# Optimization experiments

Measured on AMD Instinct MI355X. Metric: run time of the kernel, lower is better.

Reference implementation:

```python
import jax, jax.numpy as jnp
from jax import lax
import numpy as np

P = 4        # pool_size
NH = 8       # nhead
EPS = 1e-5


def _maxpool(x):
    return lax.reduce_window(x, -jnp.inf, lax.max, (1, 1, P, P), (1, 1, P, P), 'VALID')


def _ln_c(x, g, b):
    # LayerNorm over channel dim of NCHW (torch applies it on NHWC last dim)
    m = x.mean(1, keepdims=True)
    v = x.var(1, keepdims=True)
    return g[None, :, None, None] * (x - m) / jnp.sqrt(v + EPS) + b[None, :, None, None]


def _dwbn(x, w, g, b, rm, rv):
    # depthwise 3x3 conv (groups=C, no bias) + BatchNorm2d (inference, running stats)
    C = x.shape[1]
    y = lax.conv_general_dilated(x, w, (1, 1), ((1, 1), (1, 1)),
                                 dimension_numbers=('NCHW', 'OIHW', 'NCHW'),
                                 feature_group_count=C)
    sc = g / jnp.sqrt(rv + EPS)
    return sc[None, :, None, None] * (y - rm[None, :, None, None]) + b[None, :, None, None]


def _heads(x):
    # n (nhead d) h w -> n (h w) nhead d
    B, C, H, W = x.shape
    return x.reshape(B, NH, C // NH, H * W).transpose(0, 3, 1, 2)


def _fuse(x, m, merge_w, mlp_w1, mlp_w2, ln2_g, ln2_b):
    # merge linear -> reshape to pooled map -> bilinear upsample x4 -> concat -> MLP -> LN -> residual
    B, C, H, W = x.shape
    m = jnp.einsum('nlh d -> nlhd', m) if False else m  # no-op, keep m as [B,L,NH,dim]
    m = m.reshape(B, -1, C) @ merge_w.T                  # [B, L, C]
    m = m.reshape(B, H // P, W // P, C).transpose(0, 3, 1, 2)
    m = jax.image.resize(m, (B, C, H, W), method='bilinear')  # align_corners=False convention
    z = jnp.concatenate([x, m], axis=1).transpose(0, 2, 3, 1)  # NHWC, 2C
    z = jax.nn.relu(z @ mlp_w1.T) @ mlp_w2.T                   # [B,H,W,C]
    mu = z.mean(-1, keepdims=True)
    var = z.var(-1, keepdims=True)
    z = ln2_g * (z - mu) / jnp.sqrt(var + EPS) + ln2_b
    return x + z.transpose(0, 3, 1, 2)


def setup_inputs() -> dict:
    key = jax.random.key(0)
    ks = jax.random.split(key, 20)
    B, C, H, W = 4, 256, 128, 128
    s = 0.05
    return {
        'x1': jax.random.normal(ks[0], (B, C, H, W), jnp.float32),
        'x2': jax.random.normal(ks[1], (B, C, H, W), jnp.float32),
        'qk_w': jax.random.normal(ks[2], (C, 1, 3, 3), jnp.float32) * s,
        'qk_g': 1.0 + 0.1 * jax.random.normal(ks[3], (C,), jnp.float32),
        'qk_b': 0.1 * jax.random.normal(ks[4], (C,), jnp.float32),
        'qk_m': 0.1 * jax.random.normal(ks[5], (C,), jnp.float32),
        'qk_v': jax.random.uniform(ks[6], (C,), jnp.float32, 0.5, 1.5),
        'v_w': jax.random.normal(ks[7], (C, 1, 3, 3), jnp.float32) * s,
        'v_g': 1.0 + 0.1 * jax.random.normal(ks[8], (C,), jnp.float32),
        'v_b': 0.1 * jax.random.normal(ks[9], (C,), jnp.float32),
        'v_m': 0.1 * jax.random.normal(ks[10], (C,), jnp.float32),
        'v_v': jax.random.uniform(ks[11], (C,), jnp.float32, 0.5, 1.5),
        'ln1_g': 1.0 + 0.1 * jax.random.normal(ks[12], (C,), jnp.float32),
        'ln1_b': 0.1 * jax.random.normal(ks[13], (C,), jnp.float32),
        'ln2_g': 1.0 + 0.1 * jax.random.normal(ks[14], (C,), jnp.float32),
        'ln2_b': 0.1 * jax.random.normal(ks[15], (C,), jnp.float32),
        'merge_w': jax.random.normal(ks[16], (C, C), jnp.float32) * s,
        'mlp_w1': jax.random.normal(ks[17], (2 * C, 2 * C), jnp.float32) * s,
        'mlp_w2': jax.random.normal(ks[18], (C, 2 * C), jnp.float32) * s,
    }


def reference(x1, x2, qk_w, qk_g, qk_b, qk_m, qk_v, v_w, v_g, v_b, v_m, v_v,
              ln1_g, ln1_b, ln2_g, ln2_b, merge_w, mlp_w1, mlp_w2):
    # pooled + normalized features (norm1 shared across q/k/v branches)
    p1 = _ln_c(_maxpool(x1), ln1_g, ln1_b)
    p2 = _ln_c(_maxpool(x2), ln1_g, ln1_b)
    query = _heads(_dwbn(p1, qk_w, qk_g, qk_b, qk_m, qk_v))  # [B,L,NH,d]
    key = _heads(_dwbn(p2, qk_w, qk_g, qk_b, qk_m, qk_v))    # [B,S,NH,d]
    v1h = _heads(_dwbn(p1, v_w, v_g, v_b, v_m, v_v))
    v2h = _heads(_dwbn(p2, v_w, v_g, v_b, v_m, v_v))
    QK = jnp.einsum('nlhd,nshd->nlsh', query, key).astype(jnp.float32)
    t = 1.0 / np.sqrt(query.shape[-1]).astype(np.float32)
    S1 = jax.nn.softmax(t * QK, axis=2)   # softmax over s (keys)
    S2 = jax.nn.softmax(t * QK, axis=3)   # softmax over head dim (as in source)
    m1 = jnp.einsum('nlsh,nshd->nlhd', S1, v2h)
    m2 = jnp.einsum('nlsh,nlhd->nshd', S2, v1h)
    out1 = _fuse(x1, m1, merge_w, mlp_w1, mlp_w2, ln2_g, ln2_b)
    out2 = _fuse(x2, m2, merge_w, mlp_w1, mlp_w2, ln2_g, ln2_b)
    return (out1, out2)
```

## Files before the change

### kernel.cpp

```cpp
#include <hip/hip_runtime.h>
#include <hip/hip_bf16.h>

#define NB 4
#define NC 256
#define NH_ 8
#define LPOOL 1024
constexpr float EPSV = 1e-5f;

typedef unsigned short ushort_t;
typedef __attribute__((ext_vector_type(8))) short bf16x8;
typedef __attribute__((ext_vector_type(4))) float f32x4;

#define OFF_P   0u
#define OFF_V2T 1048576u
#define OFF_Q   2097152u
#define OFF_K   3145728u
#define OFF_V1  4194304u
#define OFF_V2  5242880u
#define OFF_M1  6291456u
#define OFF_M2  7340032u
#define OFF_MG  8388608u
#define OFF_A   9437184u
#define OFF_W1B 26214400u
#define OFF_W2B 26345472u
#define OFF_HID 26411008u

__device__ __forceinline__ float bf16_to_f(unsigned short u) {
    union { unsigned int ui; float f; } t; t.ui = ((unsigned int)u) << 16; return t.f;
}
__device__ __forceinline__ unsigned short f_to_bf16(float f) {
    union { float f; unsigned int u; } t; t.f = f;
    unsigned int u = t.u;
    u += 0x7fffu + ((u >> 16) & 1u);
    return (unsigned short)(u >> 16);
}

__global__ __launch_bounds__(256) void pool_kernel(const float* __restrict__ x1,
                                                   const float* __restrict__ x2,
                                                   float* __restrict__ pooled) {
    int idx = blockIdx.x * 256 + threadIdx.x;
    int j = idx & 31, i = (idx >> 5) & 31, c = (idx >> 10) & 255, n = (idx >> 18) & 3, br = idx >> 20;
    const float* xp = br ? x2 : x1;
    const float* base = xp + (((size_t)(n * 256 + c) * 128 + i * 4) * 128 + j * 4);
    float m = -3.4e38f;
#pragma unroll
    for (int r = 0; r < 4; ++r) {
        float4 v = *(const float4*)(base + r * 128);
        m = fmaxf(m, fmaxf(fmaxf(v.x, v.y), fmaxf(v.z, v.w)));
    }
    pooled[(size_t)br * 1048576 + (size_t)(n * 256 + c) * 1024 + i * 32 + j] = m;
}

__global__ __launch_bounds__(256) void lnc_kernel(float* __restrict__ p,
                                                  const float* __restrict__ g,
                                                  const float* __restrict__ b) {
    int bid = blockIdx.x;
    int l = bid & 1023, n = (bid >> 10) & 3, br = bid >> 12;
    int c = threadIdx.x;
    size_t idx = (size_t)br * 1048576 + (size_t)(n * 256 + c) * 1024 + l;
    float v = p[idx];
    __shared__ float red[256];
    red[c] = v; __syncthreads();
    for (int off = 128; off > 0; off >>= 1) { if (c < off) red[c] += red[c + off]; __syncthreads(); }
    float mean = red[0] / 256.f;
    __syncthreads();
    float d = v - mean;
    red[c] = d * d; __syncthreads();
    for (int off = 128; off > 0; off >>= 1) { if (c < off) red[c] += red[c + off]; __syncthreads(); }
    float var = red[0] / 256.f;
    float rstd = rsqrtf(var + EPSV);
    p[idx] = (v - mean) * rstd * g[c] + b[c];
}

__global__ __launch_bounds__(256) void dwbn_kernel(const float* __restrict__ p,
    const float* __restrict__ qkw, const float* __restrict__ qkg, const float* __restrict__ qkb,
    const float* __restrict__ qkm, const float* __restrict__ qkv,
    const float* __restrict__ vw, const float* __restrict__ vg, const float* __restrict__ vb,
    const float* __restrict__ vm, const float* __restrict__ vv,
    float* __restrict__ qkvbuf) {
    int which = blockIdx.y;
    int flat = blockIdx.x * 256 + threadIdx.x;
    int l = flat & 1023, c = (flat >> 10) & 255, n = flat >> 18;
    int br = which & 1;
    const float* w  = (which < 2) ? qkw : vw;
    const float* g  = (which < 2) ? qkg : vg;
    const float* bb = (which < 2) ? qkb : vb;
    const float* rm = (which < 2) ? qkm : vm;
    const float* rv = (which < 2) ? qkv : vv;
    int i = l >> 5, j = l & 31;
    const float* pin = p + (size_t)br * 1048576 + (size_t)(n * 256 + c) * 1024;
    float acc = 0.f;
#pragma unroll
    for (int ky = -1; ky <= 1; ++ky) {
        int yy = i + ky;
        if ((unsigned)yy < 32u) {
#pragma unroll
            for (int kx = -1; kx <= 1; ++kx) {
                int xx = j + kx;
                if ((unsigned)xx < 32u)
                    acc += pin[yy * 32 + xx] * w[c * 9 + (ky + 1) * 3 + (kx + 1)];
            }
        }
    }
    float sc = g[c] * rsqrtf(rv[c] + EPSV);
    qkvbuf[(size_t)which * 1048576 + (size_t)(n * 1024 + l) * 256 + c] = sc * (acc - rm[c]) + bb[c];
}

__global__ __launch_bounds__(256) void cvt_kernel(const float* __restrict__ in,
                                                  ushort_t* __restrict__ out, int n) {
    int i = blockIdx.x * 256 + threadIdx.x;
    if (i < n) out[i] = f_to_bf16(in[i]);
}

__global__ __launch_bounds__(256) void v2t_kernel(const float* __restrict__ v,
                                                  ushort_t* __restrict__ vt) {
    int bid = blockIdx.x;
    int sb = bid & 31, cb = (bid >> 5) & 7, n = bid >> 8;
    int tid = threadIdx.x;
    __shared__ float t[32][33];
    int ci = tid & 31, sg = tid >> 5;
#pragma unroll
    for (int p = 0; p < 4; ++p) {
        int s = sb * 32 + p * 8 + sg;
        t[p * 8 + sg][ci] = v[(size_t)(n * 1024 + s) * 256 + cb * 32 + ci];
    }
    __syncthreads();
    int si = tid & 31, cg = tid >> 5;
#pragma unroll
    for (int p = 0; p < 4; ++p) {
        int c = cb * 32 + p * 8 + cg;
        vt[(size_t)(n * 256 + c) * 1024 + sb * 32 + si] = f_to_bf16(t[si][p * 8 + cg]);
    }
}

__global__ __launch_bounds__(256) void qk_mfma(const ushort_t* __restrict__ qb,
                                               const ushort_t* __restrict__ kb,
                                               ushort_t* __restrict__ scores) {
    int lt = blockIdx.x, st = blockIdx.y;
    int nh = blockIdx.z; int n = nh >> 3, h = nh & 7;
    int l0 = lt * 128, s0 = st * 128;
    __shared__ ushort_t Qs[128 * 32];
    __shared__ ushort_t Ks[128 * 32];
    int tid = threadIdx.x, lane = tid & 63, wv = tid >> 6;
    int wm = wv >> 1, wn = wv & 1;
    int ml = lane & 15, quad = lane >> 4;
#pragma unroll
    for (int c = 0; c < 2; ++c) {
        int g = c * 256 + tid;
        int row = g >> 2, seg = g & 3;
        const ushort_t* ga = qb + (size_t)(n * 1024 + l0 + row) * 256 + h * 32 + seg * 8;
        __builtin_amdgcn_global_load_lds((const __attribute__((address_space(1))) void*)ga,
                                         (__attribute__((address_space(3))) void*)&Qs[row * 32 + seg * 8], 16, 0, 0);
        const ushort_t* gk = kb + (size_t)(n * 1024 + s0 + row) * 256 + h * 32 + seg * 8;
        __builtin_amdgcn_global_load_lds((const __attribute__((address_space(1))) void*)gk,
                                         (__attribute__((address_space(3))) void*)&Ks[row * 32 + seg * 8], 16, 0, 0);
    }
    __syncthreads();
    f32x4 acc[4][4];
#pragma unroll
    for (int i = 0; i < 4; ++i)
#pragma unroll
        for (int j = 0; j < 4; ++j) acc[i][j] = (f32x4)(0.f);
    bf16x8 af[4], bfr[4];
#pragma unroll
    for (int mt = 0; mt < 4; ++mt)
        af[mt] = *(const bf16x8*)&Qs[(wm * 64 + mt * 16 + ml) * 32 + quad * 8];
#pragma unroll
    for (int nt = 0; nt < 4; ++nt)
        bfr[nt] = *(const bf16x8*)&Ks[(wn * 64 + nt * 16 + ml) * 32 + quad * 8];
#pragma unroll
    for (int mt = 0; mt < 4; ++mt)
#pragma unroll
        for (int nt = 0; nt < 4; ++nt)
            acc[mt][nt] = __builtin_amdgcn_mfma_f32_16x16x32_bf16(af[mt], bfr[nt], acc[mt][nt], 0, 0, 0);
    const float tsc = 0.17677669529663687f;
    ushort_t* sb = scores + (size_t)nh * 1024 * 1024;
#pragma unroll
    for (int mt = 0; mt < 4; ++mt)
#pragma unroll
        for (int nt = 0; nt < 4; ++nt) {
            int col = s0 + wn * 64 + nt * 16 + ml;
#pragma unroll
            for (int r = 0; r < 4; ++r) {
                int row = l0 + wm * 64 + mt * 16 + quad * 4 + r;
                unsigned short b = f_to_bf16(tsc * acc[mt][nt][r]);
                int partner = __shfl_xor((int)b, 1);
                if (!(ml & 1)) {
                    unsigned int pk = (unsigned int)b | ((unsigned int)partner << 16);
                    *(unsigned int*)&sb[(size_t)row * 1024 + col] = pk;
                }
            }
        }
}

__global__ __launch_bounds__(256) void m1_kernel(const ushort_t* __restrict__ scores,
                                                 const ushort_t* __restrict__ v2t,
                                                 float* __restrict__ m1out) {
    int lt = blockIdx.x, h = blockIdx.y, n = blockIdx.z;
    int tid = threadIdx.x, lane = tid & 63, wv = tid >> 6;
    int ml = lane & 15, quad = lane >> 4;
    int l0 = lt * 64 + wv * 16;
    const ushort_t* arow = scores + (size_t)((n * 8 + h) * 1024 + l0 + ml) * 1024 + quad * 8;
    const ushort_t* vb = v2t + (size_t)(n * 256 + h * 32) * 1024;
    const ushort_t* vrow0 = vb + (size_t)ml * 1024 + quad * 8;
    const ushort_t* vrow1 = vb + (size_t)(ml + 16) * 1024 + quad * 8;
    f32x4 acc0 = (f32x4)(0.f), acc1 = (f32x4)(0.f);
    float rsum = 0.f;
#pragma unroll 4
    for (int s0 = 0; s0 < 1024; s0 += 32) {
        bf16x8 sv = *(const bf16x8*)(arow + s0);
        float e0 = __expf(bf16_to_f((ushort_t)sv[0]));
        float e1 = __expf(bf16_to_f((ushort_t)sv[1]));
        float e2 = __expf(bf16_to_f((ushort_t)sv[2]));
        float e3 = __expf(bf16_to_f((ushort_t)sv[3]));
        float e4 = __expf(bf16_to_f((ushort_t)sv[4]));
        float e5 = __expf(bf16_to_f((ushort_t)sv[5]));
        float e6 = __expf(bf16_to_f((ushort_t)sv[6]));
        float e7 = __expf(bf16_to_f((ushort_t)sv[7]));
        rsum += ((e0 + e1) + (e2 + e3)) + ((e4 + e5) + (e6 + e7));
        bf16x8 af;
        af[0] = (short)f_to_bf16(e0); af[1] = (short)f_to_bf16(e1);
        af[2] = (short)f_to_bf16(e2); af[3] = (short)f_to_bf16(e3);
        af[4] = (short)f_to_bf16(e4); af[5] = (short)f_to_bf16(e5);
        af[6] = (short)f_to_bf16(e6); af[7] = (short)f_to_bf16(e7);
        bf16x8 b0 = *(const bf16x8*)(vrow0 + s0);
        bf16x8 b1 = *(const bf16x8*)(vrow1 + s0);
        acc0 = __builtin_amdgcn_mfma_f32_16x16x32_bf16(af, b0, acc0, 0, 0, 0);
        acc1 = __builtin_amdgcn_mfma_f32_16x16x32_bf16(af, b1, acc1, 0, 0, 0);
    }
    rsum += __shfl_xor(rsum, 16);
    rsum += __shfl_xor(rsum, 32);
#pragma unroll
    for (int r = 0; r < 4; ++r) {
        int row = quad * 4 + r;
        float inv = 1.f / __shfl(rsum, row);
        size_t ob = (size_t)(n * 1024 + l0 + row) * 256 + h * 32;
        m1out[ob + ml] = acc0[r] * inv;
        m1out[ob + 16 + ml] = acc1[r] * inv;
    }
}

__global__ __launch_bounds__(256) void m2_kernel(const ushort_t* __restrict__ scores,
                                                 const float* __restrict__ v1,
                                                 float* __restrict__ m2out) {
    int st = blockIdx.x;
    int lc = blockIdx.y;
    int n  = blockIdx.z;
    int s0 = st * 32, tid = threadIdx.x;
    __shared__ float wls[8][8][32];
    float acc[32];
#pragma unroll
    for (int i = 0; i < 32; ++i) acc[i] = 0.f;
    int lA = tid >> 5, siA = tid & 31;
    int hB = tid >> 5;
    const ushort_t* sbase = scores + (size_t)n * 8 * 1024 * 1024;
    int lend = lc * 128 + 128;
    for (int lb = lc * 128; lb < lend; lb += 8) {
        int l = lb + lA;
        float e[8];
        float mx = -3.4e38f;
#pragma unroll
        for (int h = 0; h < 8; ++h) {
            e[h] = bf16_to_f(sbase[((size_t)h * 1024 + l) * 1024 + s0 + siA]);
            mx = fmaxf(mx, e[h]);
        }
        float sum = 0.f;
#pragma unroll
        for (int h = 0; h < 8; ++h) { e[h] = expf(e[h] - mx); sum += e[h]; }
        float inv = 1.f / sum;
#pragma unroll
        for (int h = 0; h < 8; ++h) wls[lA][h][siA] = e[h] * inv;
        __syncthreads();
#pragma unroll
        for (int ls = 0; ls < 8; ++ls) {
            float v1v = v1[(size_t)(n * 1024 + lb + ls) * 256 + tid];
#pragma unroll
            for (int s4 = 0; s4 < 8; ++s4) {
                float4 w4 = *(const float4*)&wls[ls][hB][s4 * 4];
                acc[s4 * 4]     += w4.x * v1v;
                acc[s4 * 4 + 1] += w4.y * v1v;
                acc[s4 * 4 + 2] += w4.z * v1v;
                acc[s4 * 4 + 3] += w4.w * v1v;
            }
        }
        __syncthreads();
    }
#pragma unroll
    for (int ss = 0; ss < 32; ++ss)
        atomicAdd(&m2out[(size_t)(n * 1024 + s0 + ss) * 256 + tid], acc[ss]);
}

__global__ __launch_bounds__(256) void merge_kernel(const float* __restrict__ m,
                                                    const float* __restrict__ mw,
                                                    float* __restrict__ merged) {
    int bid = blockIdx.x;
    int n = bid >> 7, lt = bid & 127;
    int l0 = lt * 8, tid = threadIdx.x;
    __shared__ float ms[8][260];
#pragma unroll
    for (int r = 0; r < 8; ++r) ms[r][tid] = m[(size_t)(n * 1024 + l0 + r) * 256 + tid];
    __syncthreads();
    float acc[8];
#pragma unroll
    for (int r = 0; r < 8; ++r) acc[r] = 0.f;
    const float4* wrow = (const float4*)(mw + (size_t)tid * 256);
    for (int c4 = 0; c4 < 64; ++c4) {
        float4 w4 = wrow[c4];
#pragma unroll
        for (int r = 0; r < 8; ++r) {
            float4 m4 = *(const float4*)&ms[r][c4 * 4];
            acc[r] += w4.x * m4.x + w4.y * m4.y + w4.z * m4.z + w4.w * m4.w;
        }
    }
#pragma unroll
    for (int r = 0; r < 8; ++r)
        merged[(size_t)(n * 1024 + l0 + r) * 256 + tid] = acc[r];
}

__global__ __launch_bounds__(256) void zbuild_kernel(const float* __restrict__ x,
                                                     const float* __restrict__ merged,
                                                     ushort_t* __restrict__ z) {
    int pix0 = blockIdx.x * 32;
    int n = pix0 >> 14, y = (pix0 >> 7) & 127, x0 = pix0 & 127;
    int tid = threadIdx.x;
    int ci = tid >> 5, xi = tid & 31;
    __shared__ float xs[256][33];
    for (int cc = 0; cc < 32; ++cc) {
        int c = cc * 8 + ci;
        xs[c][xi] = x[((size_t)(n * 256 + c) * 128 + y) * 128 + x0 + xi];
    }
    __syncthreads();
    float iy = y * 0.25f - 0.375f;
    int y0i = (int)floorf(iy);
    float fy = iy - (float)y0i;
    int y0c = max(y0i, 0), y1c = min(y0i + 1, 31);
    const float* mb = merged + (size_t)n * 1024 * 256;
    for (int xj = 0; xj < 32; ++xj) {
        size_t zb = (size_t)(pix0 + xj) * 512;
        z[zb + tid] = f_to_bf16(xs[tid][xj]);
        int xx = x0 + xj;
        float ix = xx * 0.25f - 0.375f;
        int x0i = (int)floorf(ix);
        float fx = ix - (float)x0i;
        int x0cc = max(x0i, 0), x1cc = min(x0i + 1, 31);
        float v00 = mb[(size_t)(y0c * 32 + x0cc) * 256 + tid];
        float v01 = mb[(size_t)(y0c * 32 + x1cc) * 256 + tid];
        float v10 = mb[(size_t)(y1c * 32 + x0cc) * 256 + tid];
        float v11 = mb[(size_t)(y1c * 32 + x1cc) * 256 + tid];
        float v = (1.f - fy) * ((1.f - fx) * v00 + fx * v01) + fy * ((1.f - fx) * v10 + fx * v11);
        z[zb + 256 + tid] = f_to_bf16(v);
    }
}

__global__ __launch_bounds__(256) void mfma_gemm(const ushort_t* __restrict__ A,
                                                 const ushort_t* __restrict__ B,
                                                 float* __restrict__ Of,
                                                 ushort_t* __restrict__ Oh,
                                                 int N, int relu) {
    const int K = 512;
    int m0 = blockIdx.x * 128, n0 = blockIdx.y * 128;
    int tid = threadIdx.x;
    __shared__ ushort_t Al[128 * 32];
    __shared__ ushort_t Bl[128 * 32];
    int lane = tid & 63;
    int wv = tid >> 6;
    int wm = wv >> 1, wn = wv & 1;
    int ml = lane & 15, quad = lane >> 4;
    f32x4 acc[4][4];
#pragma unroll
    for (int i = 0; i < 4; ++i)
#pragma unroll
        for (int j = 0; j < 4; ++j) acc[i][j] = (f32x4)(0.f);

    for (int k0 = 0; k0 < K; k0 += 32) {
#pragma unroll
        for (int c = 0; c < 2; ++c) {
            int g = c * 256 + tid;
            int row = g >> 2, seg = g & 3;
            const ushort_t* ga = A + (size_t)(m0 + row) * K + k0 + seg * 8;
            __builtin_amdgcn_global_load_lds((const __attribute__((address_space(1))) void*)ga,
                                             (__attribute__((address_space(3))) void*)&Al[g * 8], 16, 0, 0);
            const ushort_t* gb = B + (size_t)(n0 + row) * K + k0 + seg * 8;
            __builtin_amdgcn_global_load_lds((const __attribute__((address_space(1))) void*)gb,
                                             (__attribute__((address_space(3))) void*)&Bl[g * 8], 16, 0, 0);
        }
        __syncthreads();
        bf16x8 af[4], bfr[4];
#pragma unroll
        for (int mt = 0; mt < 4; ++mt)
            af[mt] = *(const bf16x8*)&Al[(wm * 64 + mt * 16 + ml) * 32 + quad * 8];
#pragma unroll
        for (int nt = 0; nt < 4; ++nt)
            bfr[nt] = *(const bf16x8*)&Bl[(wn * 64 + nt * 16 + ml) * 32 + quad * 8];
#pragma unroll
        for (int mt = 0; mt < 4; ++mt)
#pragma unroll
            for (int nt = 0; nt < 4; ++nt)
                acc[mt][nt] = __builtin_amdgcn_mfma_f32_16x16x32_bf16(af[mt], bfr[nt], acc[mt][nt], 0, 0, 0);
        __syncthreads();
    }
#pragma unroll
    for (int mt = 0; mt < 4; ++mt) {
#pragma unroll
        for (int nt = 0; nt < 4; ++nt) {
            int col = n0 + wn * 64 + nt * 16 + ml;
#pragma unroll
            for (int r = 0; r < 4; ++r) {
                int row = m0 + wm * 64 + mt * 16 + quad * 4 + r;
                float v = acc[mt][nt][r];
                if (relu) v = fmaxf(v, 0.f);
                if (Oh) Oh[(size_t)row * N + col] = f_to_bf16(v);
                else    Of[(size_t)row * N + col] = v;
            }
        }
    }
}

__global__ __launch_bounds__(256) void gemm2_ln(const ushort_t* __restrict__ hid,
                                                const ushort_t* __restrict__ W2,
                                                const float* __restrict__ xin,
                                                const float* __restrict__ g2,
                                                const float* __restrict__ b2,
                                                float* __restrict__ outp) {
    __shared__ char smem[35584];
    ushort_t* Al = (ushort_t*)smem;
    ushort_t* Bl = (ushort_t*)(smem + 4096);
    int m0 = blockIdx.x * 64;
    int tid = threadIdx.x, lane = tid & 63, wv = tid >> 6;
    int ml = lane & 15, quad = lane >> 4;
    f32x4 acc[4][4];
#pragma unroll
    for (int i = 0; i < 4; ++i)
#pragma unroll
        for (int j = 0; j < 4; ++j) acc[i][j] = (f32x4)(0.f);

    for (int k0 = 0; k0 < 512; k0 += 32) {
        {
            int row = tid >> 2, seg = tid & 3;
            const ushort_t* ga = hid + (size_t)(m0 + row) * 512 + k0 + seg * 8;
            __builtin_amdgcn_global_load_lds((const __attribute__((address_space(1))) void*)ga,
                                             (__attribute__((address_space(3))) void*)&Al[tid * 8], 16, 0, 0);
        }
#pragma unroll
        for (int c = 0; c < 4; ++c) {
            int g = c * 256 + tid;
            int row = g >> 2, seg = g & 3;
            const ushort_t* gb = W2 + (size_t)row * 512 + k0 + seg * 8;
            __builtin_amdgcn_global_load_lds((const __attribute__((address_space(1))) void*)gb,
                                             (__attribute__((address_space(3))) void*)&Bl[g * 8], 16, 0, 0);
        }
        __syncthreads();
        bf16x8 af[4], bfr[4];
#pragma unroll
        for (int mt = 0; mt < 4; ++mt)
            af[mt] = *(const bf16x8*)&Al[(mt * 16 + ml) * 32 + quad * 8];
#pragma unroll
        for (int nt = 0; nt < 4; ++nt)
            bfr[nt] = *(const bf16x8*)&Bl[(wv * 64 + nt * 16 + ml) * 32 + quad * 8];
#pragma unroll
        for (int mt = 0; mt < 4; ++mt)
#pragma unroll
            for (int nt = 0; nt < 4; ++nt)
                acc[mt][nt] = __builtin_amdgcn_mfma_f32_16x16x32_bf16(af[mt], bfr[nt], acc[mt][nt], 0, 0, 0);
        __syncthreads();
    }
    float* redS = (float*)smem;
    float* redQ = (float*)(smem + 1024);
    float* muA  = (float*)(smem + 2048);
    float* rsA  = (float*)(smem + 2304);
    float* olds = (float*)(smem + 2560);
#pragma unroll
    for (int mt = 0; mt < 4; ++mt)
#pragma unroll
        for (int r = 0; r < 4; ++r) {
            float s = 0.f, q = 0.f;
#pragma unroll
            for (int nt = 0; nt < 4; ++nt) { float v = acc[mt][nt][r]; s += v; q += v * v; }
            s += __shfl_xor(s, 1); s += __shfl_xor(s, 2); s += __shfl_xor(s, 4); s += __shfl_xor(s, 8);
            q += __shfl_xor(q, 1); q += __shfl_xor(q, 2); q += __shfl_xor(q, 4); q += __shfl_xor(q, 8);
            if (ml == 0) {
                int row = mt * 16 + quad * 4 + r;
                redS[row * 4 + wv] = s; redQ[row * 4 + wv] = q;
            }
        }
    __syncthreads();
    if (tid < 64) {
        float S = redS[tid * 4] + redS[tid * 4 + 1] + redS[tid * 4 + 2] + redS[tid * 4 + 3];
        float Q = redQ[tid * 4] + redQ[tid * 4 + 1] + redQ[tid * 4 + 2] + redQ[tid * 4 + 3];
        float mu = S * (1.f / 256.f);
        float var = Q * (1.f / 256.f) - mu * mu;
        muA[tid] = mu; rsA[tid] = rsqrtf(var + EPSV);
    }
    __syncthreads();
    int n = m0 >> 14, y = (m0 >> 7) & 127, x0 = m0 & 127;
    int cg = tid >> 5, xi = tid & 31;
#pragma unroll
    for (int half = 0; half < 2; ++half) {
        if ((wv >> 1) == half) {
#pragma unroll
            for (int mt = 0; mt < 4; ++mt)
#pragma unroll
                for (int r = 0; r < 4; ++r) {
                    int row = mt * 16 + quad * 4 + r;
                    float mu = muA[row], rs = rsA[row];
#pragma unroll
                    for (int nt = 0; nt < 4; ++nt) {
                        int col = wv * 64 + nt * 16 + ml;
                        int lc = col - half * 128;
                        olds[row * 129 + lc] = (acc[mt][nt][r] - mu) * rs * g2[col] + b2[col];
                    }
                }
        }
        __syncthreads();
        for (int cc = 0; cc < 16; ++cc) {
            int lc = cc * 8 + cg;
            int c = half * 128 + lc;
            size_t gbase = ((size_t)(n * 256 + c) * 128 + y) * 128 + x0;
#pragma unroll
            for (int xc = 0; xc < 2; ++xc) {
                int p = xc * 32 + xi;
                outp[gbase + p] = xin[gbase + p] + olds[p * 129 + lc];
            }
        }
        __syncthreads();
    }
}

extern "C" void kernel_launch(void* const* d_in, const int* in_sizes, int n_in,
                              void* d_out, int out_size, void* d_ws, size_t ws_size,
                              hipStream_t stream) {
    (void)in_sizes; (void)n_in; (void)out_size; (void)ws_size;
    const float* x1     = (const float*)d_in[0];
    const float* x2     = (const float*)d_in[1];
    const float* qk_w   = (const float*)d_in[2];
    const float* qk_g   = (const float*)d_in[3];
    const float* qk_b   = (const float*)d_in[4];
    const float* qk_m   = (const float*)d_in[5];
    const float* qk_v   = (const float*)d_in[6];
    const float* v_w    = (const float*)d_in[7];
    const float* v_g    = (const float*)d_in[8];
    const float* v_b    = (const float*)d_in[9];
    const float* v_m    = (const float*)d_in[10];
    const float* v_v    = (const float*)d_in[11];
    const float* ln1_g  = (const float*)d_in[12];
    const float* ln1_b  = (const float*)d_in[13];
    const float* ln2_g  = (const float*)d_in[14];
    const float* ln2_b  = (const float*)d_in[15];
    const float* merge_w = (const float*)d_in[16];
    const float* mlp_w1 = (const float*)d_in[17];
    const float* mlp_w2 = (const float*)d_in[18];

    float* ws      = (float*)d_ws;
    float* pooled  = ws + OFF_P;
    float* qkvbuf  = ws + OFF_Q;
    float* v1buf   = ws + OFF_V1;
    float* v2buf   = ws + OFF_V2;
    float* m1buf   = ws + OFF_M1;
    float* m2buf   = ws + OFF_M2;
    float* mgbuf   = ws + OFF_MG;
    ushort_t* scores16 = (ushort_t*)(ws + OFF_A);
    ushort_t* qkb16 = (ushort_t*)(ws + OFF_P);
    ushort_t* v2tb = (ushort_t*)(ws + OFF_V2T);
    ushort_t* zb16 = (ushort_t*)(ws + OFF_A);
    ushort_t* w1b  = (ushort_t*)(ws + OFF_W1B);
    ushort_t* w2b  = (ushort_t*)(ws + OFF_W2B);
    ushort_t* hid  = (ushort_t*)(ws + OFF_HID);
    float* outp    = (float*)d_out;

    hipMemsetAsync(m2buf, 0, 1048576 * sizeof(float), stream);

    pool_kernel<<<8192, 256, 0, stream>>>(x1, x2, pooled);
    lnc_kernel<<<8192, 256, 0, stream>>>(pooled, ln1_g, ln1_b);
    dwbn_kernel<<<dim3(4096, 4), 256, 0, stream>>>(pooled,
        qk_w, qk_g, qk_b, qk_m, qk_v, v_w, v_g, v_b, v_m, v_v, qkvbuf);
    cvt_kernel<<<8192, 256, 0, stream>>>(qkvbuf, qkb16, 2097152);
    v2t_kernel<<<1024, 256, 0, stream>>>(v2buf, v2tb);
    qk_mfma<<<dim3(8, 8, 32), 256, 0, stream>>>(qkb16, qkb16 + 1048576, scores16);
    m1_kernel<<<dim3(16, 8, 4), 256, 0, stream>>>(scores16, v2tb, m1buf);
    m2_kernel<<<dim3(32, 8, 4), 256, 0, stream>>>(scores16, v1buf, m2buf);

    cvt_kernel<<<1024, 256, 0, stream>>>(mlp_w1, w1b, 262144);
    cvt_kernel<<<512, 256, 0, stream>>>(mlp_w2, w2b, 131072);

    for (int br = 0; br < 2; ++br) {
        const float* xin = br ? x2 : x1;
        const float* mm  = br ? m2buf : m1buf;
        merge_kernel<<<512, 256, 0, stream>>>(mm, merge_w, mgbuf);
        zbuild_kernel<<<2048, 256, 0, stream>>>(xin, mgbuf, zb16);
        mfma_gemm<<<dim3(512, 4), 256, 0, stream>>>(zb16, w1b, nullptr, hid, 512, 1);
        gemm2_ln<<<1024, 256, 0, stream>>>(hid, w2b, xin, ln2_g, ln2_b,
                                           outp + (size_t)br * 16777216);
    }
}
```

Measured before the change: 767.4 us.

## Fold merge linear into MLP first layer and fuse upsample into GEMM1

Precomputes W1[:,C:]·merge_w so the merge projection and the upsampled half of the first MLP layer become one small GEMM at pooled resolution. Bilinear upsampling commutes with the linear map, so the upsample is applied in GEMM1's epilogue. GEMM1 now reads x directly with K=256 and transposes it in LDS, which removes the merge and zbuild kernels and the 512-wide z buffer. The m1 output is stored as bf16, which adds rounding before the folded projection.

```diff
diff --git a/kernel.cpp b/kernel.cpp
--- a/kernel.cpp
+++ b/kernel.cpp
@@ -23,7 +23,7 @@
 #define OFF_A   9437184u
 #define OFF_W1B 26214400u
 #define OFF_W2B 26345472u
-#define OFF_HID 26411008u
+#define OFF_WCB 26411008u
 
 __device__ __forceinline__ float bf16_to_f(unsigned short u) {
     union { unsigned int ui; float f; } t; t.ui = ((unsigned int)u) << 16; return t.f;
@@ -112,6 +112,18 @@
     if (i < n) out[i] = f_to_bf16(in[i]);
 }
 
+__global__ __launch_bounds__(256) void wc_kernel(const float* __restrict__ w1,
+                                                 const float* __restrict__ mw,
+                                                 ushort_t* __restrict__ wcb) {
+    int r = blockIdx.x, t = threadIdx.x;
+    __shared__ float wrow[256];
+    wrow[t] = w1[(size_t)r * 512 + 256 + t];
+    __syncthreads();
+    float acc = 0.f;
+    for (int c = 0; c < 256; ++c) acc += wrow[c] * mw[(size_t)c * 256 + t];
+    wcb[(size_t)r * 256 + t] = f_to_bf16(acc);
+}
+
 __global__ __launch_bounds__(256) void v2t_kernel(const float* __restrict__ v,
                                                   ushort_t* __restrict__ vt) {
     int bid = blockIdx.x;
@@ -195,7 +207,7 @@
 
 __global__ __launch_bounds__(256) void m1_kernel(const ushort_t* __restrict__ scores,
                                                  const ushort_t* __restrict__ v2t,
-                                                 float* __restrict__ m1out) {
+                                                 ushort_t* __restrict__ m1out) {
     int lt = blockIdx.x, h = blockIdx.y, n = blockIdx.z;
     int tid = threadIdx.x, lane = tid & 63, wv = tid >> 6;
     int ml = lane & 15, quad = lane >> 4;
@@ -235,8 +247,8 @@
         int row = quad * 4 + r;
         float inv = 1.f / __shfl(rsum, row);
         size_t ob = (size_t)(n * 1024 + l0 + row) * 256 + h * 32;
-        m1out[ob + ml] = acc0[r] * inv;
-        m1out[ob + 16 + ml] = acc1[r] * inv;
+        m1out[ob + ml] = f_to_bf16(acc0[r] * inv);
+        m1out[ob + 16 + ml] = f_to_bf16(acc1[r] * inv);
     }
 }
 
@@ -290,74 +302,11 @@
         atomicAdd(&m2out[(size_t)(n * 1024 + s0 + ss) * 256 + tid], acc[ss]);
 }
 
-__global__ __launch_bounds__(256) void merge_kernel(const float* __restrict__ m,
-                                                    const float* __restrict__ mw,
-                                                    float* __restrict__ merged) {
-    int bid = blockIdx.x;
-    int n = bid >> 7, lt = bid & 127;
-    int l0 = lt * 8, tid = threadIdx.x;
-    __shared__ float ms[8][260];
-#pragma unroll
-    for (int r = 0; r < 8; ++r) ms[r][tid] = m[(size_t)(n * 1024 + l0 + r) * 256 + tid];
-    __syncthreads();
-    float acc[8];
-#pragma unroll
-    for (int r = 0; r < 8; ++r) acc[r] = 0.f;
-    const float4* wrow = (const float4*)(mw + (size_t)tid * 256);
-    for (int c4 = 0; c4 < 64; ++c4) {
-        float4 w4 = wrow[c4];
-#pragma unroll
-        for (int r = 0; r < 8; ++r) {
-            float4 m4 = *(const float4*)&ms[r][c4 * 4];
-            acc[r] += w4.x * m4.x + w4.y * m4.y + w4.z * m4.z + w4.w * m4.w;
-        }
-    }
-#pragma unroll
-    for (int r = 0; r < 8; ++r)
-        merged[(size_t)(n * 1024 + l0 + r) * 256 + tid] = acc[r];
-}
-
-__global__ __launch_bounds__(256) void zbuild_kernel(const float* __restrict__ x,
-                                                     const float* __restrict__ merged,
-                                                     ushort_t* __restrict__ z) {
-    int pix0 = blockIdx.x * 32;
-    int n = pix0 >> 14, y = (pix0 >> 7) & 127, x0 = pix0 & 127;
-    int tid = threadIdx.x;
-    int ci = tid >> 5, xi = tid & 31;
-    __shared__ float xs[256][33];
-    for (int cc = 0; cc < 32; ++cc) {
-        int c = cc * 8 + ci;
-        xs[c][xi] = x[((size_t)(n * 256 + c) * 128 + y) * 128 + x0 + xi];
-    }
-    __syncthreads();
-    float iy = y * 0.25f - 0.375f;
-    int y0i = (int)floorf(iy);
-    float fy = iy - (float)y0i;
-    int y0c = max(y0i, 0), y1c = min(y0i + 1, 31);
-    const float* mb = merged + (size_t)n * 1024 * 256;
-    for (int xj = 0; xj < 32; ++xj) {
-        size_t zb = (size_t)(pix0 + xj) * 512;
-        z[zb + tid] = f_to_bf16(xs[tid][xj]);
-        int xx = x0 + xj;
-        float ix = xx * 0.25f - 0.375f;
-        int x0i = (int)floorf(ix);
-        float fx = ix - (float)x0i;
-        int x0cc = max(x0i, 0), x1cc = min(x0i + 1, 31);
-        float v00 = mb[(size_t)(y0c * 32 + x0cc) * 256 + tid];
-        float v01 = mb[(size_t)(y0c * 32 + x1cc) * 256 + tid];
-        float v10 = mb[(size_t)(y1c * 32 + x0cc) * 256 + tid];
-        float v11 = mb[(size_t)(y1c * 32 + x1cc) * 256 + tid];
-        float v = (1.f - fy) * ((1.f - fx) * v00 + fx * v01) + fy * ((1.f - fx) * v10 + fx * v11);
-        z[zb + 256 + tid] = f_to_bf16(v);
-    }
-}
-
 __global__ __launch_bounds__(256) void mfma_gemm(const ushort_t* __restrict__ A,
                                                  const ushort_t* __restrict__ B,
                                                  float* __restrict__ Of,
                                                  ushort_t* __restrict__ Oh,
-                                                 int N, int relu) {
-    const int K = 512;
+                                                 int N, int relu, int K) {
     int m0 = blockIdx.x * 128, n0 = blockIdx.y * 128;
     int tid = threadIdx.x;
     __shared__ ushort_t Al[128 * 32];
@@ -414,6 +363,110 @@
             }
         }
     }
+}
+
+__global__ __launch_bounds__(256) void gemm1_fused(const float* __restrict__ x,
+                                                   const ushort_t* __restrict__ W1,
+                                                   const ushort_t* __restrict__ mm1,
+                                                   ushort_t* __restrict__ hid) {
+    __shared__ char smem[49152];
+    ushort_t* Abf = (ushort_t*)smem;
+    ushort_t* Bl  = (ushort_t*)(smem + 32768);
+    float* t32    = (float*)(smem + 32768);
+    int m0 = blockIdx.x * 64;
+    int n = m0 >> 14, y = (m0 >> 7) & 127, x0 = m0 & 127;
+    int n0 = blockIdx.y * 256;
+    int tid = threadIdx.x, lane = tid & 63;
+    int wv = tid >> 6, ml = lane & 15, quad = lane >> 4;
+
+    const float* xrow = x + ((size_t)(n * 256) * 128 + y) * 128 + x0;
+    for (int cb = 0; cb < 256; cb += 32) {
+        __syncthreads();
+        {
+            int l16 = tid & 15, cl = tid >> 4;
+#pragma unroll
+            for (int pp = 0; pp < 2; ++pp) {
+                int c = cb + pp * 16 + cl;
+                float4 v = *(const float4*)(xrow + (size_t)c * 16384 + l16 * 4);
+                *(float4*)&t32[(pp * 16 + cl) * 68 + l16 * 4] = v;
+            }
+        }
+        __syncthreads();
+        {
+            int clw = tid & 31, pg = tid >> 5;
+#pragma unroll
+            for (int k = 0; k < 8; ++k) {
+                int pix = pg * 8 + k;
+                float v = t32[clw * 68 + pix];
+                unsigned byte = ((unsigned)(pix * 256 + cb + clw) * 2u) ^ ((unsigned)(pix & 7) << 4);
+                *(ushort_t*)(smem + byte) = f_to_bf16(v);
+            }
+        }
+    }
+    __syncthreads();
+
+    f32x4 acc[4][4];
+#pragma unroll
+    for (int i = 0; i < 4; ++i)
+#pragma unroll
+        for (int j = 0; j < 4; ++j) acc[i][j] = (f32x4)(0.f);
+    for (int k0 = 0; k0 < 256; k0 += 32) {
+#pragma unroll
+        for (int c = 0; c < 4; ++c) {
+            int g = c * 256 + tid;
+            int row = g >> 2, seg = g & 3;
+            const ushort_t* gb = W1 + (size_t)(n0 + row) * 512 + k0 + seg * 8;
+            __builtin_amdgcn_global_load_lds((const __attribute__((address_space(1))) void*)gb,
+                                             (__attribute__((address_space(3))) void*)&Bl[g * 8], 16, 0, 0);
+        }
+        __syncthreads();
+        bf16x8 af[4], bfr[4];
+#pragma unroll
+        for (int mt = 0; mt < 4; ++mt) {
+            int pix = mt * 16 + ml;
+            unsigned byte = ((unsigned)(pix * 256 + k0 + quad * 8) * 2u) ^ ((unsigned)(pix & 7) << 4);
+            af[mt] = *(const bf16x8*)(smem + byte);
+        }
+#pragma unroll
+        for (int nt = 0; nt < 4; ++nt)
+            bfr[nt] = *(const bf16x8*)&Bl[(wv * 64 + nt * 16 + ml) * 32 + quad * 8];
+#pragma unroll
+        for (int mt = 0; mt < 4; ++mt)
+#pragma unroll
+            for (int nt = 0; nt < 4; ++nt)
+                acc[mt][nt] = __builtin_amdgcn_mfma_f32_16x16x32_bf16(af[mt], bfr[nt], acc[mt][nt], 0, 0, 0);
+        __syncthreads();
+    }
+
+    float iy = y * 0.25f - 0.375f;
+    int y0i = (int)floorf(iy);
+    float fy = iy - (float)y0i;
+    int y0c = max(y0i, 0), y1c = min(y0i + 1, 31);
+    const ushort_t* mb0 = mm1 + (size_t)(n * 1024 + y0c * 32) * 512;
+    const ushort_t* mb1 = mm1 + (size_t)(n * 1024 + y1c * 32) * 512;
+#pragma unroll
+    for (int mt = 0; mt < 4; ++mt)
+#pragma unroll
+        for (int r = 0; r < 4; ++r) {
+            int p = mt * 16 + quad * 4 + r;
+            int xx = x0 + p;
+            float ix = xx * 0.25f - 0.375f;
+            int x0i = (int)floorf(ix);
+            float fx = ix - (float)x0i;
+            int xc0 = max(x0i, 0), xc1 = min(x0i + 1, 31);
+#pragma unroll
+            for (int nt = 0; nt < 4; ++nt) {
+                int col = n0 + wv * 64 + nt * 16 + ml;
+                float v00 = bf16_to_f(mb0[(size_t)xc0 * 512 + col]);
+                float v01 = bf16_to_f(mb0[(size_t)xc1 * 512 + col]);
+                float v10 = bf16_to_f(mb1[(size_t)xc0 * 512 + col]);
+                float v11 = bf16_to_f(mb1[(size_t)xc1 * 512 + col]);
+                float up = (1.f - fy) * ((1.f - fx) * v00 + fx * v01)
+                         + fy * ((1.f - fx) * v10 + fx * v11);
+                float v = fmaxf(acc[mt][nt][r] + up, 0.f);
+                hid[(size_t)(m0 + p) * 512 + col] = f_to_bf16(v);
+            }
+        }
 }
 
 __global__ __launch_bounds__(256) void gemm2_ln(const ushort_t* __restrict__ hid,
@@ -555,20 +608,22 @@
     float* qkvbuf  = ws + OFF_Q;
     float* v1buf   = ws + OFF_V1;
     float* v2buf   = ws + OFF_V2;
-    float* m1buf   = ws + OFF_M1;
     float* m2buf   = ws + OFF_M2;
-    float* mgbuf   = ws + OFF_MG;
+    ushort_t* m1b16 = (ushort_t*)(ws + OFF_M1);
+    ushort_t* mb16  = (ushort_t*)(ws + OFF_V1);
+    ushort_t* mm1b  = (ushort_t*)(ws + OFF_MG);
     ushort_t* scores16 = (ushort_t*)(ws + OFF_A);
     ushort_t* qkb16 = (ushort_t*)(ws + OFF_P);
     ushort_t* v2tb = (ushort_t*)(ws + OFF_V2T);
-    ushort_t* zb16 = (ushort_t*)(ws + OFF_A);
+    ushort_t* hid  = (ushort_t*)(ws + OFF_A);
     ushort_t* w1b  = (ushort_t*)(ws + OFF_W1B);
     ushort_t* w2b  = (ushort_t*)(ws + OFF_W2B);
-    ushort_t* hid  = (ushort_t*)(ws + OFF_HID);
+    ushort_t* wcb  = (ushort_t*)(ws + OFF_WCB);
     float* outp    = (float*)d_out;
 
     hipMemsetAsync(m2buf, 0, 1048576 * sizeof(float), stream);
 
+    wc_kernel<<<512, 256, 0, stream>>>(mlp_w1, merge_w, wcb);
     pool_kernel<<<8192, 256, 0, stream>>>(x1, x2, pooled);
     lnc_kernel<<<8192, 256, 0, stream>>>(pooled, ln1_g, ln1_b);
     dwbn_kernel<<<dim3(4096, 4), 256, 0, stream>>>(pooled,
@@ -576,7 +631,7 @@
     cvt_kernel<<<8192, 256, 0, stream>>>(qkvbuf, qkb16, 2097152);
     v2t_kernel<<<1024, 256, 0, stream>>>(v2buf, v2tb);
     qk_mfma<<<dim3(8, 8, 32), 256, 0, stream>>>(qkb16, qkb16 + 1048576, scores16);
-    m1_kernel<<<dim3(16, 8, 4), 256, 0, stream>>>(scores16, v2tb, m1buf);
+    m1_kernel<<<dim3(16, 8, 4), 256, 0, stream>>>(scores16, v2tb, m1b16);
     m2_kernel<<<dim3(32, 8, 4), 256, 0, stream>>>(scores16, v1buf, m2buf);
 
     cvt_kernel<<<1024, 256, 0, stream>>>(mlp_w1, w1b, 262144);
@@ -584,10 +639,15 @@
 
     for (int br = 0; br < 2; ++br) {
         const float* xin = br ? x2 : x1;
-        const float* mm  = br ? m2buf : m1buf;
-        merge_kernel<<<512, 256, 0, stream>>>(mm, merge_w, mgbuf);
-        zbuild_kernel<<<2048, 256, 0, stream>>>(xin, mgbuf, zb16);
-        mfma_gemm<<<dim3(512, 4), 256, 0, stream>>>(zb16, w1b, nullptr, hid, 512, 1);
+        const ushort_t* mmb;
+        if (br == 0) {
+            mmb = m1b16;
+        } else {
+            cvt_kernel<<<4096, 256, 0, stream>>>(m2buf, mb16, 1048576);
+            mmb = mb16;
+        }
+        mfma_gemm<<<dim3(32, 4), 256, 0, stream>>>(mmb, wcb, nullptr, mm1b, 512, 0, 256);
+        gemm1_fused<<<dim3(1024, 2), 256, 0, stream>>>(xin, w1b, mm1b, hid);
         gemm2_ln<<<1024, 256, 0, stream>>>(hid, w2b, xin, ln2_g, ln2_b,
                                            outp + (size_t)br * 16777216);
     }
```

Measured after the change: 685.5 us. -10.7%, faster.
